# Performance work log

Measured on AMD Instinct MI355X. Metric: run time of the kernel, lower is better.

The kernel has to match this reference:

```python
import jax, jax.numpy as jnp
import numpy as np

N = 100000   # nodes
E = 1200000  # edges
G = 128      # graphs in batch
VOCAB = 10000
D = 64       # node_emb_dim
H = 64       # hidden_dim
R = 64       # readout_dim
BN_EPS = 1e-5


def _mlp_bn(h, W1, b1, g, be, W2, b2):
    # PyG MLP([in,H,H], act='ELU'): Linear -> BatchNorm(eval, running mean=0, var=1) -> ELU -> Linear
    h = h @ W1 + b1
    h = h * (g / jnp.sqrt(1.0 + BN_EPS)) + be
    h = jax.nn.elu(h)
    return h @ W2 + b2


def _gin(h, src, dst, W1, b1, g, be, W2, b2):
    # GINConv(eps=0): nn((1+0)*x_i + sum_{j->i} x_j)
    agg = jax.ops.segment_sum(h[src], dst, num_segments=N)
    return _mlp_bn(h + agg, W1, b1, g, be, W2, b2)


def setup_inputs() -> dict:
    key = jax.random.key(0)
    ks = iter(jax.random.split(key, 40))
    inp = {}
    inp["x"] = jax.random.randint(next(ks), (N, 1), 0, VOCAB)
    inp["edge_index"] = jax.random.randint(next(ks), (2, E), 0, N)
    inp["batch"] = jnp.sort(jax.random.randint(next(ks), (N,), 0, G))
    # embedding init: normal with std = dim**-0.5 (matches initialize_parameters)
    inp["emb"] = jax.random.normal(next(ks), (VOCAB, D), jnp.float32) * (D ** -0.5)

    def lin(k, fi, fo):
        return jax.random.normal(k, (fi, fo), jnp.float32) / np.sqrt(fi)

    for tag, fi in (("a", D), ("b", H), ("c", H)):
        inp[f"W1{tag}"] = lin(next(ks), fi, H)
        inp[f"b1{tag}"] = jnp.zeros((H,), jnp.float32)
        inp[f"g{tag}"] = jnp.ones((H,), jnp.float32)
        inp[f"be{tag}"] = jnp.zeros((H,), jnp.float32)
        inp[f"W2{tag}"] = lin(next(ks), H, H)
        inp[f"b2{tag}"] = jnp.zeros((H,), jnp.float32)

    inp["Wr1"] = lin(next(ks), H, H)
    inp["br1"] = jnp.zeros((H,), jnp.float32)
    inp["Wr2"] = lin(next(ks), H, R)
    inp["br2"] = jnp.zeros((R,), jnp.float32)
    inp["Wo"] = lin(next(ks), R, 1)
    inp["bo"] = jnp.zeros((1,), jnp.float32)
    return inp


def reference(x, edge_index, batch, emb,
              W1a, b1a, ga, bea, W2a, b2a,
              W1b, b1b, gb, beb, W2b, b2b,
              W1c, b1c, gc, bec, W2c, b2c,
              Wr1, br1, Wr2, br2, Wo, bo):
    # eval mode: dropout layers are identity
    src, dst = edge_index[0], edge_index[1]
    h = emb[x[:, 0]]                                        # [N, D]
    h = jax.nn.elu(_gin(h, src, dst, W1a, b1a, ga, bea, W2a, b2a))
    h = jax.nn.elu(_gin(h, src, dst, W1b, b1b, gb, beb, W2b, b2b))
    h = jax.nn.elu(_gin(h, src, dst, W1c, b1c, gc, bec, W2c, b2c))
    # global mean pool over graphs
    sums = jax.ops.segment_sum(h, batch, num_segments=G)    # [G, H]
    cnts = jax.ops.segment_sum(jnp.ones((N,), h.dtype), batch, num_segments=G)
    pooled = sums / jnp.maximum(cnts, 1.0)[:, None]
    # readout MLP (norm=None, dropout inactive in eval): Lin -> ELU -> Lin
    r = jax.nn.elu(pooled @ Wr1 + br1) @ Wr2 + br2
    return r @ Wo + bo                                      # [G, 1]
```

## Files before the change

### kernel.cpp

```cpp
#include <hip/hip_runtime.h>
#include <hip/hip_bf16.h>

#define N_NODES 100000
#define N_EDGES 1200000
#define G_GRAPHS 128
#define CAP 64
#define AP 68
#define SLICE_N 12500

__global__ void scatter_k(const int* __restrict__ ei, int* __restrict__ cnt,
                          int* __restrict__ adj) {
    int slice = blockIdx.x & 7;
    int e = (blockIdx.x >> 3) * 256 + threadIdx.x;
    if (e >= N_EDGES) return;
    int s = ei[e];
    int d = ei[N_EDGES + e];
    s = min(max(s, 0), N_NODES - 1);
    d = min(max(d, 0), N_NODES - 1);
    if (d / SLICE_N != slice) return;
    int pos = atomicAdd(&cnt[d], 1);
    if (pos < CAP) adj[d * CAP + pos] = s;
}

__global__ void pad_k(int* __restrict__ cnt, int* __restrict__ adj) {
    int n = blockIdx.x * 256 + threadIdx.x;
    if (n >= N_NODES) return;
    int c = min(cnt[n], CAP);
    int p = min((c + 7) & ~7, CAP);
    for (int i = c; i < p; ++i) adj[n * CAP + i] = N_NODES;
    cnt[n] = p;
}

__global__ void embed_k(const int* __restrict__ x, const float4* __restrict__ emb,
                        float4* __restrict__ h) {
    int t = blockIdx.x * 256 + threadIdx.x;
    if (t >= N_NODES * 16) return;
    int n = t >> 4, q = t & 15;
    h[n * 16 + q] = emb[x[n] * 16 + q];
}

__device__ __forceinline__ void f4add(float4& a, const float4 b) {
    a.x += b.x; a.y += b.y; a.z += b.z; a.w += b.w;
}

__global__ void agg_k(const float4* __restrict__ h, const int* __restrict__ adj,
                      const int* __restrict__ cnt, float4* __restrict__ agg) {
    int t = blockIdx.x * 256 + threadIdx.x;
    int n = t >> 4, q = t & 15;
    if (n >= N_NODES) return;
    int deg = cnt[n];
    const int4* al4 = (const int4*)(adj + n * CAP);
    float4 a0 = h[n * 16 + q];
    float4 a1 = make_float4(0.f, 0.f, 0.f, 0.f);
    float4 a2 = a1, a3 = a1, a4 = a1, a5 = a1, a6 = a1, a7 = a1;
    int d8 = deg >> 3;
    for (int i = 0; i < d8; ++i) {
        int4 sa = al4[2 * i];
        int4 sb = al4[2 * i + 1];
        float4 v0 = h[sa.x * 16 + q];
        float4 v1 = h[sa.y * 16 + q];
        float4 v2 = h[sa.z * 16 + q];
        float4 v3 = h[sa.w * 16 + q];
        float4 v4 = h[sb.x * 16 + q];
        float4 v5 = h[sb.y * 16 + q];
        float4 v6 = h[sb.z * 16 + q];
        float4 v7 = h[sb.w * 16 + q];
        f4add(a0, v0); f4add(a1, v1); f4add(a2, v2); f4add(a3, v3);
        f4add(a4, v4); f4add(a5, v5); f4add(a6, v6); f4add(a7, v7);
    }
    f4add(a0, a1); f4add(a2, a3); f4add(a4, a5); f4add(a6, a7);
    f4add(a0, a2); f4add(a4, a6); f4add(a0, a4);
    agg[n * 16 + q] = a0;
}

__device__ __forceinline__ float elu(float v) { return v > 0.f ? v : expm1f(v); }

#define FMA16(comp, wv)                                                        \
    acc[0][0] += av0.comp * wv.x; acc[0][1] += av0.comp * wv.y;                \
    acc[0][2] += av0.comp * wv.z; acc[0][3] += av0.comp * wv.w;                \
    acc[1][0] += av1.comp * wv.x; acc[1][1] += av1.comp * wv.y;                \
    acc[1][2] += av1.comp * wv.z; acc[1][3] += av1.comp * wv.w;                \
    acc[2][0] += av2.comp * wv.x; acc[2][1] += av2.comp * wv.y;                \
    acc[2][2] += av2.comp * wv.z; acc[2][3] += av2.comp * wv.w;                \
    acc[3][0] += av3.comp * wv.x; acc[3][1] += av3.comp * wv.y;                \
    acc[3][2] += av3.comp * wv.z; acc[3][3] += av3.comp * wv.w;

__device__ __forceinline__ void mm64(const float* __restrict__ A,
                                     const float* __restrict__ Ws,
                                     float acc[4][4], int tr, int tc) {
    #pragma unroll 2
    for (int k4 = 0; k4 < 16; ++k4) {
        float4 av0 = *(const float4*)(A + (tr * 4 + 0) * AP + k4 * 4);
        float4 av1 = *(const float4*)(A + (tr * 4 + 1) * AP + k4 * 4);
        float4 av2 = *(const float4*)(A + (tr * 4 + 2) * AP + k4 * 4);
        float4 av3 = *(const float4*)(A + (tr * 4 + 3) * AP + k4 * 4);
        {
            float4 wv = *(const float4*)(Ws + (k4 * 4 + 0) * 64 + tc * 4);
            FMA16(x, wv)
        }
        {
            float4 wv = *(const float4*)(Ws + (k4 * 4 + 1) * 64 + tc * 4);
            FMA16(y, wv)
        }
        {
            float4 wv = *(const float4*)(Ws + (k4 * 4 + 2) * 64 + tc * 4);
            FMA16(z, wv)
        }
        {
            float4 wv = *(const float4*)(Ws + (k4 * 4 + 3) * 64 + tc * 4);
            FMA16(w, wv)
        }
    }
}

__global__ void __launch_bounds__(256, 4) mlp_k(const float* __restrict__ agg,
    float* __restrict__ h,
    const float* __restrict__ W1, const float* __restrict__ b1,
    const float* __restrict__ g,  const float* __restrict__ be,
    const float* __restrict__ W2, const float* __restrict__ b2) {
    __shared__ float At[64 * AP];
    __shared__ float Ws1[4096];
    __shared__ float Ws2[4096];
    __shared__ float sc1[64], ep1[64], ep2[64];
    int tid = threadIdx.x;
    int n0 = blockIdx.x * 64;

    for (int idx = tid; idx < 1024; idx += 256) {
        ((float4*)Ws1)[idx] = ((const float4*)W1)[idx];
        ((float4*)Ws2)[idx] = ((const float4*)W2)[idx];
    }
    if (tid < 64) {
        const float inv = rsqrtf(1.0f + 1e-5f);
        float s = g[tid] * inv;
        sc1[tid] = s;
        ep1[tid] = b1[tid] * s + be[tid];
        ep2[tid] = b2[tid];
    }
    {
        int r = tid >> 4, q = tid & 15;
        #pragma unroll
        for (int p = 0; p < 4; ++p) {
            int rr = p * 16 + r;
            int n = n0 + rr;
            float4 v = (n < N_NODES) ? ((const float4*)agg)[n * 16 + q]
                                     : make_float4(0.f, 0.f, 0.f, 0.f);
            *(float4*)(At + rr * AP + q * 4) = v;
        }
    }
    __syncthreads();

    int tr = tid >> 4, tc = tid & 15;
    float acc[4][4];
    #pragma unroll
    for (int e = 0; e < 4; ++e)
        #pragma unroll
        for (int j = 0; j < 4; ++j) acc[e][j] = 0.f;

    mm64(At, Ws1, acc, tr, tc);
    __syncthreads();
    #pragma unroll
    for (int e = 0; e < 4; ++e) {
        float4 o;
        o.x = elu(acc[e][0] * sc1[tc * 4 + 0] + ep1[tc * 4 + 0]);
        o.y = elu(acc[e][1] * sc1[tc * 4 + 1] + ep1[tc * 4 + 1]);
        o.z = elu(acc[e][2] * sc1[tc * 4 + 2] + ep1[tc * 4 + 2]);
        o.w = elu(acc[e][3] * sc1[tc * 4 + 3] + ep1[tc * 4 + 3]);
        *(float4*)(At + (tr * 4 + e) * AP + tc * 4) = o;
    }
    __syncthreads();
    #pragma unroll
    for (int e = 0; e < 4; ++e)
        #pragma unroll
        for (int j = 0; j < 4; ++j) acc[e][j] = 0.f;

    mm64(At, Ws2, acc, tr, tc);
    #pragma unroll
    for (int e = 0; e < 4; ++e) {
        int n = n0 + tr * 4 + e;
        if (n < N_NODES) {
            float4 o;
            o.x = elu(acc[e][0] + ep2[tc * 4 + 0]);
            o.y = elu(acc[e][1] + ep2[tc * 4 + 1]);
            o.z = elu(acc[e][2] + ep2[tc * 4 + 2]);
            o.w = elu(acc[e][3] + ep2[tc * 4 + 3]);
            ((float4*)h)[n * 16 + tc] = o;
        }
    }
}

__global__ void pool_k(const float4* __restrict__ h, const int* __restrict__ batch,
                       float4* __restrict__ pooled) {
    int gph = blockIdx.x;
    int tid = threadIdx.x;
    int lo = 0, hi = N_NODES;
    while (lo < hi) { int mid = (lo + hi) >> 1; if (batch[mid] < gph) lo = mid + 1; else hi = mid; }
    int start = lo;
    hi = N_NODES;
    while (lo < hi) { int mid = (lo + hi) >> 1; if (batch[mid] < gph + 1) lo = mid + 1; else hi = mid; }
    int end = lo;
    int q = tid & 15, r = tid >> 4;
    float4 acc = make_float4(0.f, 0.f, 0.f, 0.f);
    for (int n = start + r; n < end; n += 16) {
        float4 v = h[n * 16 + q];
        acc.x += v.x; acc.y += v.y; acc.z += v.z; acc.w += v.w;
    }
    __shared__ float4 red[256];
    red[tid] = acc;
    __syncthreads();
    for (int s = 8; s > 0; s >>= 1) {
        if (r < s) {
            float4 o = red[(r + s) * 16 + q];
            float4 m = red[r * 16 + q];
            m.x += o.x; m.y += o.y; m.z += o.z; m.w += o.w;
            red[r * 16 + q] = m;
        }
        __syncthreads();
    }
    if (r == 0) {
        float invc = 1.0f / fmaxf((float)(end - start), 1.0f);
        float4 m = red[q];
        m.x *= invc; m.y *= invc; m.z *= invc; m.w *= invc;
        pooled[gph * 16 + q] = m;
    }
}

__global__ void __launch_bounds__(256) head_k(const float* __restrict__ pooled,
    const float* __restrict__ Wr1, const float* __restrict__ br1,
    const float* __restrict__ Wr2, const float* __restrict__ br2,
    const float* __restrict__ Wo,  const float* __restrict__ bo,
    float* __restrict__ out) {
    __shared__ float ylds[4][64];
    int wid = threadIdx.x >> 6, j = threadIdx.x & 63;
    int gph = blockIdx.x * 4 + wid;
    float acc = 0.f;
    #pragma unroll 8
    for (int k = 0; k < 64; ++k)
        acc += pooled[gph * 64 + k] * Wr1[k * 64 + j];
    float yv = acc + br1[j];
    ylds[wid][j] = elu(yv);
    __syncthreads();
    float acc2 = 0.f;
    #pragma unroll 8
    for (int k = 0; k < 64; ++k)
        acc2 += ylds[wid][k] * Wr2[k * 64 + j];
    float p = (acc2 + br2[j]) * Wo[j];
    #pragma unroll
    for (int off = 32; off > 0; off >>= 1) p += __shfl_down(p, off);
    if (j == 0) out[gph] = bo[0] + p;
}

extern "C" void kernel_launch(void* const* d_in, const int* in_sizes, int n_in,
                              void* d_out, int out_size, void* d_ws, size_t ws_size,
                              hipStream_t stream) {
    const int*   x     = (const int*)d_in[0];
    const int*   ei    = (const int*)d_in[1];
    const int*   batch = (const int*)d_in[2];
    const float* emb   = (const float*)d_in[3];
    const float* P[24];
    for (int i = 0; i < 24; ++i) P[i] = (const float*)d_in[4 + i];

    char* ws = (char*)d_ws;
    float* h      = (float*)(ws + 0);
    float* agg    = (float*)(ws + 26000000);
    int*   adj    = (int*)  (ws + 52000000);
    int*   cnt    = (int*)  (ws + 78000000);
    float* pooled = (float*)(ws + 78400000);

    hipMemsetAsync(cnt, 0, N_NODES * sizeof(int), stream);
    hipMemsetAsync(h + N_NODES * 64, 0, 64 * sizeof(float), stream);
    scatter_k<<<8 * ((N_EDGES + 255) / 256), 256, 0, stream>>>(ei, cnt, adj);
    pad_k<<<(N_NODES + 255) / 256, 256, 0, stream>>>(cnt, adj);
    embed_k<<<(N_NODES * 16 + 255) / 256, 256, 0, stream>>>(x, (const float4*)emb, (float4*)h);
    for (int L = 0; L < 3; ++L) {
        const float* const* p = P + 6 * L;
        agg_k<<<(N_NODES * 16 + 255) / 256, 256, 0, stream>>>(
            (const float4*)h, adj, cnt, (float4*)agg);
        mlp_k<<<(N_NODES + 63) / 64, 256, 0, stream>>>(
            agg, h, p[0], p[1], p[2], p[3], p[4], p[5]);
    }
    pool_k<<<G_GRAPHS, 256, 0, stream>>>((const float4*)h, batch, (float4*)pooled);
    head_k<<<32, 256, 0, stream>>>(pooled, P[18], P[19], P[20], P[21], P[22], P[23],
                                   (float*)d_out);
}
```

Before: 463.3 us.

## Fuse neighbor aggregation into MLP kernel with ping-pong feature buffers

Moves the gather-sum over neighbors into the MLP kernel's tile-load phase, so the separate aggregation kernel and its write and re-read of the agg buffer go away. Because the kernel now reads neighbors while writing outputs, features ping-pong between two buffers, and the final layer's output lands in hB. The padding kernel is removed and tail lanes are masked to a zero sentinel row instead. Weight shared memory is halved by reusing one buffer for W1 then W2, which may allow more blocks per CU. The cost is a gather-heavy, irregular load phase inside the compute kernel, where each block handles only 64 nodes with 16 threads per node.

Result: faster. 419.2 us (-9.5%).

```diff
diff --git a/kernel.cpp b/kernel.cpp
--- a/kernel.cpp
+++ b/kernel.cpp
@@ -22,15 +22,6 @@
     if (pos < CAP) adj[d * CAP + pos] = s;
 }
 
-__global__ void pad_k(int* __restrict__ cnt, int* __restrict__ adj) {
-    int n = blockIdx.x * 256 + threadIdx.x;
-    if (n >= N_NODES) return;
-    int c = min(cnt[n], CAP);
-    int p = min((c + 7) & ~7, CAP);
-    for (int i = c; i < p; ++i) adj[n * CAP + i] = N_NODES;
-    cnt[n] = p;
-}
-
 __global__ void embed_k(const int* __restrict__ x, const float4* __restrict__ emb,
                         float4* __restrict__ h) {
     int t = blockIdx.x * 256 + threadIdx.x;
@@ -41,36 +32,6 @@
 
 __device__ __forceinline__ void f4add(float4& a, const float4 b) {
     a.x += b.x; a.y += b.y; a.z += b.z; a.w += b.w;
-}
-
-__global__ void agg_k(const float4* __restrict__ h, const int* __restrict__ adj,
-                      const int* __restrict__ cnt, float4* __restrict__ agg) {
-    int t = blockIdx.x * 256 + threadIdx.x;
-    int n = t >> 4, q = t & 15;
-    if (n >= N_NODES) return;
-    int deg = cnt[n];
-    const int4* al4 = (const int4*)(adj + n * CAP);
-    float4 a0 = h[n * 16 + q];
-    float4 a1 = make_float4(0.f, 0.f, 0.f, 0.f);
-    float4 a2 = a1, a3 = a1, a4 = a1, a5 = a1, a6 = a1, a7 = a1;
-    int d8 = deg >> 3;
-    for (int i = 0; i < d8; ++i) {
-        int4 sa = al4[2 * i];
-        int4 sb = al4[2 * i + 1];
-        float4 v0 = h[sa.x * 16 + q];
-        float4 v1 = h[sa.y * 16 + q];
-        float4 v2 = h[sa.z * 16 + q];
-        float4 v3 = h[sa.w * 16 + q];
-        float4 v4 = h[sb.x * 16 + q];
-        float4 v5 = h[sb.y * 16 + q];
-        float4 v6 = h[sb.z * 16 + q];
-        float4 v7 = h[sb.w * 16 + q];
-        f4add(a0, v0); f4add(a1, v1); f4add(a2, v2); f4add(a3, v3);
-        f4add(a4, v4); f4add(a5, v5); f4add(a6, v6); f4add(a7, v7);
-    }
-    f4add(a0, a1); f4add(a2, a3); f4add(a4, a5); f4add(a6, a7);
-    f4add(a0, a2); f4add(a4, a6); f4add(a0, a4);
-    agg[n * 16 + q] = a0;
 }
 
 __device__ __forceinline__ float elu(float v) { return v > 0.f ? v : expm1f(v); }
@@ -113,22 +74,21 @@
     }
 }
 
-__global__ void __launch_bounds__(256, 4) mlp_k(const float* __restrict__ agg,
-    float* __restrict__ h,
+__global__ void __launch_bounds__(256, 4) mlp_k(const float* __restrict__ hin,
+    float* __restrict__ hout, const int* __restrict__ adj,
+    const int* __restrict__ cnt,
     const float* __restrict__ W1, const float* __restrict__ b1,
     const float* __restrict__ g,  const float* __restrict__ be,
     const float* __restrict__ W2, const float* __restrict__ b2) {
     __shared__ float At[64 * AP];
-    __shared__ float Ws1[4096];
-    __shared__ float Ws2[4096];
+    __shared__ float Wbuf[4096];
     __shared__ float sc1[64], ep1[64], ep2[64];
     int tid = threadIdx.x;
     int n0 = blockIdx.x * 64;
-
-    for (int idx = tid; idx < 1024; idx += 256) {
-        ((float4*)Ws1)[idx] = ((const float4*)W1)[idx];
-        ((float4*)Ws2)[idx] = ((const float4*)W2)[idx];
-    }
+    const float4* h4 = (const float4*)hin;
+
+    for (int idx = tid; idx < 1024; idx += 256)
+        ((float4*)Wbuf)[idx] = ((const float4*)W1)[idx];
     if (tid < 64) {
         const float inv = rsqrtf(1.0f + 1e-5f);
         float s = g[tid] * inv;
@@ -142,9 +102,41 @@
         for (int p = 0; p < 4; ++p) {
             int rr = p * 16 + r;
             int n = n0 + rr;
-            float4 v = (n < N_NODES) ? ((const float4*)agg)[n * 16 + q]
-                                     : make_float4(0.f, 0.f, 0.f, 0.f);
-            *(float4*)(At + rr * AP + q * 4) = v;
+            float4 a0 = make_float4(0.f, 0.f, 0.f, 0.f);
+            if (n < N_NODES) {
+                a0 = h4[n * 16 + q];
+                int deg = min(cnt[n], CAP);
+                const int4* al4 = (const int4*)(adj + n * CAP);
+                float4 a1 = make_float4(0.f, 0.f, 0.f, 0.f);
+                float4 a2 = a1, a3 = a1, a4 = a1, a5 = a1, a6 = a1, a7 = a1;
+                int g8 = (deg + 7) >> 3;
+                for (int i = 0; i < g8; ++i) {
+                    int4 sa = al4[2 * i];
+                    int4 sb = al4[2 * i + 1];
+                    int base = i * 8;
+                    int s0 = (base + 0 < deg) ? sa.x : N_NODES;
+                    int s1 = (base + 1 < deg) ? sa.y : N_NODES;
+                    int s2 = (base + 2 < deg) ? sa.z : N_NODES;
+                    int s3 = (base + 3 < deg) ? sa.w : N_NODES;
+                    int s4 = (base + 4 < deg) ? sb.x : N_NODES;
+                    int s5 = (base + 5 < deg) ? sb.y : N_NODES;
+                    int s6 = (base + 6 < deg) ? sb.z : N_NODES;
+                    int s7 = (base + 7 < deg) ? sb.w : N_NODES;
+                    float4 v0 = h4[s0 * 16 + q];
+                    float4 v1 = h4[s1 * 16 + q];
+                    float4 v2 = h4[s2 * 16 + q];
+                    float4 v3 = h4[s3 * 16 + q];
+                    float4 v4 = h4[s4 * 16 + q];
+                    float4 v5 = h4[s5 * 16 + q];
+                    float4 v6 = h4[s6 * 16 + q];
+                    float4 v7 = h4[s7 * 16 + q];
+                    f4add(a0, v0); f4add(a1, v1); f4add(a2, v2); f4add(a3, v3);
+                    f4add(a4, v4); f4add(a5, v5); f4add(a6, v6); f4add(a7, v7);
+                }
+                f4add(a0, a1); f4add(a2, a3); f4add(a4, a5); f4add(a6, a7);
+                f4add(a0, a2); f4add(a4, a6); f4add(a0, a4);
+            }
+            *(float4*)(At + rr * AP + q * 4) = a0;
         }
     }
     __syncthreads();
@@ -156,7 +148,7 @@
         #pragma unroll
         for (int j = 0; j < 4; ++j) acc[e][j] = 0.f;
 
-    mm64(At, Ws1, acc, tr, tc);
+    mm64(At, Wbuf, acc, tr, tc);
     __syncthreads();
     #pragma unroll
     for (int e = 0; e < 4; ++e) {
@@ -167,13 +159,15 @@
         o.w = elu(acc[e][3] * sc1[tc * 4 + 3] + ep1[tc * 4 + 3]);
         *(float4*)(At + (tr * 4 + e) * AP + tc * 4) = o;
     }
+    for (int idx = tid; idx < 1024; idx += 256)
+        ((float4*)Wbuf)[idx] = ((const float4*)W2)[idx];
     __syncthreads();
     #pragma unroll
     for (int e = 0; e < 4; ++e)
         #pragma unroll
         for (int j = 0; j < 4; ++j) acc[e][j] = 0.f;
 
-    mm64(At, Ws2, acc, tr, tc);
+    mm64(At, Wbuf, acc, tr, tc);
     #pragma unroll
     for (int e = 0; e < 4; ++e) {
         int n = n0 + tr * 4 + e;
@@ -183,7 +177,7 @@
             o.y = elu(acc[e][1] + ep2[tc * 4 + 1]);
             o.z = elu(acc[e][2] + ep2[tc * 4 + 2]);
             o.w = elu(acc[e][3] + ep2[tc * 4 + 3]);
-            ((float4*)h)[n * 16 + tc] = o;
+            ((float4*)hout)[n * 16 + tc] = o;
         }
     }
 }
@@ -260,25 +254,25 @@
     for (int i = 0; i < 24; ++i) P[i] = (const float*)d_in[4 + i];
 
     char* ws = (char*)d_ws;
-    float* h      = (float*)(ws + 0);
-    float* agg    = (float*)(ws + 26000000);
+    float* hA     = (float*)(ws + 0);
+    float* hB     = (float*)(ws + 26000000);
     int*   adj    = (int*)  (ws + 52000000);
     int*   cnt    = (int*)  (ws + 78000000);
     float* pooled = (float*)(ws + 78400000);
 
     hipMemsetAsync(cnt, 0, N_NODES * sizeof(int), stream);
-    hipMemsetAsync(h + N_NODES * 64, 0, 64 * sizeof(float), stream);
+    hipMemsetAsync(hA + N_NODES * 64, 0, 64 * sizeof(float), stream);
+    hipMemsetAsync(hB + N_NODES * 64, 0, 64 * sizeof(float), stream);
     scatter_k<<<8 * ((N_EDGES + 255) / 256), 256, 0, stream>>>(ei, cnt, adj);
-    pad_k<<<(N_NODES + 255) / 256, 256, 0, stream>>>(cnt, adj);
-    embed_k<<<(N_NODES * 16 + 255) / 256, 256, 0, stream>>>(x, (const float4*)emb, (float4*)h);
+    embed_k<<<(N_NODES * 16 + 255) / 256, 256, 0, stream>>>(x, (const float4*)emb, (float4*)hA);
     for (int L = 0; L < 3; ++L) {
         const float* const* p = P + 6 * L;
-        agg_k<<<(N_NODES * 16 + 255) / 256, 256, 0, stream>>>(
-            (const float4*)h, adj, cnt, (float4*)agg);
+        const float* hin = (L & 1) ? hB : hA;
+        float* hout      = (L & 1) ? hA : hB;
         mlp_k<<<(N_NODES + 63) / 64, 256, 0, stream>>>(
-            agg, h, p[0], p[1], p[2], p[3], p[4], p[5]);
-    }
-    pool_k<<<G_GRAPHS, 256, 0, stream>>>((const float4*)h, batch, (float4*)pooled);
+            hin, hout, adj, cnt, p[0], p[1], p[2], p[3], p[4], p[5]);
+    }
+    pool_k<<<G_GRAPHS, 256, 0, stream>>>((const float4*)hB, batch, (float4*)pooled);
     head_k<<<32, 256, 0, stream>>>(pooled, P[18], P[19], P[20], P[21], P[22], P[23],
                                    (float*)d_out);
 }
```
